# Kernel optimization log

Measured on AMD Instinct MI355X. Metric: run time of the kernel, lower is better.

The kernel has to match this reference:

```python
import jax, jax.numpy as jnp
import numpy as np

B, D_IN, D_OUT, N_CACHE = 2048, 1024, 512, 50000


def setup_inputs() -> dict:
    key = jax.random.key(0)
    k1, k2, k3, k4, k5 = jax.random.split(key, 5)
    scale = 1.0 / np.sqrt(D_IN)
    return {
        "x": jax.random.normal(k1, (B, D_IN), dtype=jnp.float32),
        "W": jax.random.normal(k2, (D_OUT, D_IN), dtype=jnp.float32) * scale,
        "b": jax.random.normal(k3, (D_OUT,), dtype=jnp.float32) * 0.01,
        "cache_image_features": jax.random.normal(k4, (N_CACHE, D_OUT), dtype=jnp.float32),
        "cache_text_features": jax.random.normal(k5, (N_CACHE, D_OUT), dtype=jnp.float32),
        "beta": jnp.ones((1,), dtype=jnp.float32),
        "alpha": jnp.ones((1,), dtype=jnp.float32),
    }


def reference(x, W, b, cache_image_features, cache_text_features, beta, alpha):
    # projected_x = x @ W.T + b  -> [B, D_OUT]
    projected_x = jnp.einsum('bi,oi->bo', x, W) + b
    # similarity over cached image features -> [B, N_CACHE]
    similarity = jnp.einsum('bo,no->bn', projected_x, cache_image_features)
    weights = jax.nn.softmax(beta * similarity, axis=-1)
    # retrieve from cached text features -> [B, D_OUT]
    retrieved = jnp.einsum('bn,no->bo', weights, cache_text_features)
    return projected_x + alpha * retrieved
```

## Files before the change

kernel.cpp:

```cpp
#include <hip/hip_runtime.h>
#include <hip/hip_bf16.h>
#include <math.h>

typedef _Float16 f16;
typedef __attribute__((ext_vector_type(8))) _Float16 f16x8;
typedef __attribute__((ext_vector_type(4))) float f32x4;
typedef __attribute__((ext_vector_type(16))) float f32x16;
typedef __attribute__((ext_vector_type(4))) unsigned int u32x4;
typedef __attribute__((ext_vector_type(2))) unsigned int u32x2;

#define MFMA16(A, B, C) __builtin_amdgcn_mfma_f32_16x16x32_f16(A, B, C, 0, 0, 0)
#define MFMA32(A, B, C) __builtin_amdgcn_mfma_f32_32x32x16_f16(A, B, C, 0, 0, 0)
#define AS1 __attribute__((address_space(1)))
#define AS3 __attribute__((address_space(3)))

__device__ __forceinline__ void gld16(const char* g, char* l) {
  __builtin_amdgcn_global_load_lds((const AS1 void*)g, (AS3 void*)l, 16, 0, 0);
}

__device__ __forceinline__ unsigned pk2(float a, float b) {
  f16 x = (f16)a, y = (f16)b;
  unsigned short ux = __builtin_bit_cast(unsigned short, x);
  unsigned short uy = __builtin_bit_cast(unsigned short, y);
  return (unsigned)ux | ((unsigned)uy << 16);
}

namespace {
constexpr int kB = 2048;
constexpr int kNch = 16, kChunk = 3125, kNit = 98;
constexpr int kKRows = 50176;
constexpr int kVStride = 3200;
constexpr size_t WS_PROJ = 0;
constexpr size_t WS_QHI  = WS_PROJ + (size_t)2048 * 512 * 4;
constexpr size_t WS_M    = WS_QHI + (size_t)2048 * 512 * 2;
constexpr size_t WS_L    = WS_M + (size_t)kNch * kB * 4;
constexpr size_t WS_PV   = WS_L + (size_t)kNch * kB * 4;
constexpr size_t WS_K16  = WS_PV + (size_t)kNch * kB * 512 * 2;
constexpr size_t WS_VT   = WS_K16 + (size_t)kKRows * 512 * 2;
constexpr int LDS_K0 = 0, LDS_K1 = 33280;
constexpr int LDS_V0 = 66560, LDS_V1 = 99328;
constexpr int LDS_SXP = 132096;
constexpr int LDS_FAC = 148480;
constexpr int LDS_SZ  = 148992;
}

__global__ __launch_bounds__(256) void convk_kernel(const float* __restrict__ src,
                                                    f16* __restrict__ dst) {
  const size_t e = ((size_t)blockIdx.x * 256 + threadIdx.x) * 8;
  const int row = (int)(e >> 9);
  float4 a = make_float4(0.f, 0.f, 0.f, 0.f), b = a;
  if (row < 50000) {
    a = *(const float4*)(src + e);
    b = *(const float4*)(src + e + 4);
  }
  f16x8 h;
  h[0] = (f16)a.x; h[1] = (f16)a.y; h[2] = (f16)a.z; h[3] = (f16)a.w;
  h[4] = (f16)b.x; h[5] = (f16)b.y; h[6] = (f16)b.z; h[7] = (f16)b.w;
  *(f16x8*)(dst + e) = h;
}

__global__ __launch_bounds__(256) void transv_kernel(const float* __restrict__ Vf,
                                                     f16* __restrict__ Vt) {
  __shared__ float tile[64][65];
  const int kt = blockIdx.x, colt = blockIdx.y, ch = blockIdx.z;
  const int t = threadIdx.x;
  const int kbase = kt * 64, col0 = colt * 64;
  {
    const int key = t >> 2, cseg = (t & 3) * 16;
    const int kk = kbase + key;
    float4 v0 = make_float4(0.f, 0.f, 0.f, 0.f), v1 = v0, v2 = v0, v3 = v0;
    if (kk < kChunk) {
      const float* s = Vf + (size_t)(ch * kChunk + kk) * 512 + col0 + cseg;
      v0 = *(const float4*)(s);
      v1 = *(const float4*)(s + 4);
      v2 = *(const float4*)(s + 8);
      v3 = *(const float4*)(s + 12);
    }
    float* tr = &tile[key][cseg];
    tr[0] = v0.x;  tr[1] = v0.y;  tr[2] = v0.z;  tr[3] = v0.w;
    tr[4] = v1.x;  tr[5] = v1.y;  tr[6] = v1.z;  tr[7] = v1.w;
    tr[8] = v2.x;  tr[9] = v2.y;  tr[10] = v2.z; tr[11] = v2.w;
    tr[12] = v3.x; tr[13] = v3.y; tr[14] = v3.z; tr[15] = v3.w;
  }
  __syncthreads();
  {
    const int col = t >> 2, kw = (t & 3) * 16;
    f16x8 h0, h1;
    #pragma unroll
    for (int u = 0; u < 8; u++) h0[u] = (f16)tile[kw + u][col];
    #pragma unroll
    for (int u = 0; u < 8; u++) h1[u] = (f16)tile[kw + 8 + u][col];
    f16* d = Vt + ((size_t)ch * 512 + col0 + col) * kVStride + kbase + kw;
    *(f16x8*)(d) = h0;
    *(f16x8*)(d + 8) = h1;
  }
}

__global__ __launch_bounds__(256) void gemm1_kernel(
    const float* __restrict__ x, const float* __restrict__ W,
    const float* __restrict__ bias, float* __restrict__ proj,
    f16* __restrict__ qhi)
{
  __shared__ f16 xh[2][64][40], xl[2][64][40], wh[2][64][40], wl[2][64][40];
  const int t = threadIdx.x;
  const int lane = t & 63, w = t >> 6;
  const int wr = w >> 1, wc = w & 1;
  const int g = lane >> 4, j = lane & 15;
  const int m0 = blockIdx.x * 64, n0 = blockIdx.y * 64;
  const int srow = t >> 2;
  const int soff = (t & 3) * 8;

  const f32x4 fzero = {0.f, 0.f, 0.f, 0.f};
  f32x4 acc[2][2], acc2[2][2];
  #pragma unroll
  for (int a = 0; a < 2; a++)
    #pragma unroll
    for (int bb = 0; bb < 2; bb++) { acc[a][bb] = fzero; acc2[a][bb] = fzero; }

  auto stage = [&](int k0s, int buf) {
    const float* xs  = x + (size_t)(m0 + srow) * 1024 + k0s + soff;
    const float* wsr = W + (size_t)(n0 + srow) * 1024 + k0s + soff;
    f16x8 hx, lx, hw, lw;
    #pragma unroll
    for (int i = 0; i < 8; i++) {
      float v = xs[i];
      f16 h = (f16)v;
      hx[i] = h;
      lx[i] = (f16)((v - (float)h) * 2048.0f);
      float u = wsr[i];
      f16 hu = (f16)u;
      hw[i] = hu;
      lw[i] = (f16)((u - (float)hu) * 2048.0f);
    }
    *(f16x8*)&xh[buf][srow][soff] = hx;
    *(f16x8*)&xl[buf][srow][soff] = lx;
    *(f16x8*)&wh[buf][srow][soff] = hw;
    *(f16x8*)&wl[buf][srow][soff] = lw;
  };

  stage(0, 0);
  for (int ks = 0; ks < 32; ks++) {
    __syncthreads();
    if (ks < 31) stage((ks + 1) * 32, (ks + 1) & 1);
    const int buf = ks & 1;
    f16x8 ah[2], al[2], bh[2], bl[2];
    #pragma unroll
    for (int mf = 0; mf < 2; mf++) {
      const int r = wr * 32 + mf * 16 + j;
      ah[mf] = *(const f16x8*)&xh[buf][r][g * 8];
      al[mf] = *(const f16x8*)&xl[buf][r][g * 8];
      const int c = wc * 32 + mf * 16 + j;
      bh[mf] = *(const f16x8*)&wh[buf][c][g * 8];
      bl[mf] = *(const f16x8*)&wl[buf][c][g * 8];
    }
    #pragma unroll
    for (int mf = 0; mf < 2; mf++)
      #pragma unroll
      for (int nf = 0; nf < 2; nf++) {
        acc[mf][nf]  = MFMA16(ah[mf], bh[nf], acc[mf][nf]);
        acc2[mf][nf] = MFMA16(ah[mf], bl[nf], acc2[mf][nf]);
        acc2[mf][nf] = MFMA16(al[mf], bh[nf], acc2[mf][nf]);
      }
  }

  #pragma unroll
  for (int mf = 0; mf < 2; mf++)
    #pragma unroll
    for (int nf = 0; nf < 2; nf++)
      #pragma unroll
      for (int r = 0; r < 4; r++) {
        const int m = m0 + wr * 32 + mf * 16 + g * 4 + r;
        const int n = n0 + wc * 32 + nf * 16 + j;
        float p = acc[mf][nf][r] + acc2[mf][nf][r] * (1.0f / 2048.0f) + bias[n];
        proj[(size_t)m * 512 + n] = p;
        qhi[(size_t)m * 512 + n] = (f16)p;
      }
}

__global__ __launch_bounds__(512, 2) void attn_kernel(
    const f16* __restrict__ K16, const f16* __restrict__ Vt16,
    const f16* __restrict__ qhi_ws, const float* __restrict__ beta_p,
    float* __restrict__ m_part, float* __restrict__ l_part,
    f16* __restrict__ pvn)
{
  extern __shared__ char smem[];
  const int t = threadIdx.x, lane = t & 63, w = t >> 6;
  const int c = lane & 31, h = lane >> 5;
  const int qb = w & 3, dh = w >> 2;
  const int ch = blockIdx.x & 15, qt = blockIdx.x >> 4;
  const int q0 = qt * 128;
  const float beta = beta_p[0];

  char* const Kb0 = smem + LDS_K0;
  char* const Kb1 = smem + LDS_K1;
  char* const Vb0 = smem + LDS_V0;
  char* const Vb1 = smem + LDS_V1;
  char* const SxP = smem + LDS_SXP + qb * 4096;
  float* const facl = (float*)(smem + LDS_FAC);

  f16x8 Qf[16];
  {
    const f16* qsrc = qhi_ws + (size_t)(q0 + qb * 32 + c) * 512 + dh * 256 + h * 8;
    #pragma unroll
    for (int i = 0; i < 16; i++) Qf[i] = *(const f16x8*)(qsrc + i * 16);
  }

  const char* const Kg = (const char*)K16 + (size_t)(ch * kChunk) * 1024;
  const char* const Vg = (const char*)Vt16 + (size_t)ch * 512 * (kVStride * 2);
  const int vlo = (((lane & 3) ^ ((lane >> 2) & 3)) << 4);

  auto stageK = [&](int it, char* dstbuf) {
    const char* src = Kg + (size_t)(it * 32 + w * 4) * 1024 + lane * 16;
    char* dst = dstbuf + (w * 4) * 1040 + lane * 16;
    #pragma unroll
    for (int u = 0; u < 4; u++) gld16(src + u * 1024, dst + u * 1040);
  };
  auto stageV = [&](int it, char* dstbuf) {
    const char* src = Vg + (size_t)(w * 64 + (lane >> 2)) * (kVStride * 2) + it * 64 + vlo;
    char* dst = dstbuf + (w * 64) * 64 + lane * 16;
    #pragma unroll
    for (int u = 0; u < 4; u++)
      gld16(src + (size_t)(u * 16) * (kVStride * 2), dst + u * 1024);
  };

  const int kroff = c * 1040 + dh * 512 + h * 16;
  const int vroff0 = (dh * 256 + c) * 64 + ((h * 16) ^ ((c & 3) << 4));
  const int vroff1 = (dh * 256 + c) * 64 + ((32 + h * 16) ^ ((c & 3) << 4));

  f32x16 O[8];
  #pragma unroll
  for (int nf = 0; nf < 8; nf++)
    #pragma unroll
    for (int r = 0; r < 16; r++) O[nf][r] = 0.f;
  float mrow = -INFINITY, lrow = 0.f;

  stageK(0, Kb0);
  stageV(0, Vb0);
  asm volatile("s_waitcnt vmcnt(0)" ::: "memory");
  __builtin_amdgcn_s_barrier();

  for (int it = 0; it < kNit; it++) {
    const int p = it & 1;
    char* const Kp = p ? Kb1 : Kb0;
    char* const Vp = p ? Vb1 : Vb0;
    if (it + 1 < kNit) {
      stageK(it + 1, p ? Kb0 : Kb1);
      stageV(it + 1, p ? Vb0 : Vb1);
    }

    f32x16 S;
    #pragma unroll
    for (int r = 0; r < 16; r++) S[r] = 0.f;
    const char* ka = Kp + kroff;
    __builtin_amdgcn_s_setprio(1);
    #pragma unroll
    for (int i = 0; i < 16; i++) {
      f16x8 a = *(const f16x8*)(ka + i * 32);
      S = MFMA32(a, Qf[i], S);
    }
    __builtin_amdgcn_s_setprio(0);

    if (dh == 1) {
      f32x4 v0 = {S[0], S[1], S[2], S[3]};
      f32x4 v1 = {S[4], S[5], S[6], S[7]};
      f32x4 v2 = {S[8], S[9], S[10], S[11]};
      f32x4 v3 = {S[12], S[13], S[14], S[15]};
      *(f32x4*)(SxP + 0 * 1024 + lane * 16) = v0;
      *(f32x4*)(SxP + 1 * 1024 + lane * 16) = v1;
      *(f32x4*)(SxP + 2 * 1024 + lane * 16) = v2;
      *(f32x4*)(SxP + 3 * 1024 + lane * 16) = v3;
    }
    asm volatile("s_waitcnt lgkmcnt(0)" ::: "memory");
    __builtin_amdgcn_s_barrier();

    u32x4 B0, B1;
    float fc;
    if (dh == 0) {
      #pragma unroll
      for (int cc = 0; cc < 4; cc++) {
        f32x4 v = *(const f32x4*)(SxP + cc * 1024 + lane * 16);
        S[4 * cc + 0] += v.x; S[4 * cc + 1] += v.y;
        S[4 * cc + 2] += v.z; S[4 * cc + 3] += v.w;
      }
      #pragma unroll
      for (int r = 0; r < 16; r++) S[r] *= beta;
      if (it == kNit - 1) {
        #pragma unroll
        for (int r = 0; r < 16; r++) {
          const int key = it * 32 + (r & 3) + 8 * (r >> 2) + 4 * h;
          if (key >= kChunk) S[r] = -INFINITY;
        }
      }
      float pm = S[0];
      #pragma unroll
      for (int r = 1; r < 16; r++) pm = fmaxf(pm, S[r]);
      pm = fmaxf(pm, __shfl_xor(pm, 32));
      const float mn = fmaxf(mrow, pm);
      fc = __expf(mrow - mn);
      mrow = mn;
      float pr[16], rs = 0.f;
      #pragma unroll
      for (int r = 0; r < 16; r++) { pr[r] = __expf(S[r] - mn); rs += pr[r]; }
      rs += __shfl_xor(rs, 32);
      lrow = lrow * fc + rs;
      unsigned pA0 = pk2(pr[0], pr[1]),  pA1 = pk2(pr[2], pr[3]);
      unsigned pB0 = pk2(pr[4], pr[5]),  pB1 = pk2(pr[6], pr[7]);
      unsigned pC0 = pk2(pr[8], pr[9]),  pC1 = pk2(pr[10], pr[11]);
      unsigned pD0 = pk2(pr[12], pr[13]), pD1 = pk2(pr[14], pr[15]);
      unsigned sA0 = __shfl_xor(pA0, 32), sA1 = __shfl_xor(pA1, 32);
      unsigned sB0 = __shfl_xor(pB0, 32), sB1 = __shfl_xor(pB1, 32);
      unsigned sC0 = __shfl_xor(pC0, 32), sC1 = __shfl_xor(pC1, 32);
      unsigned sD0 = __shfl_xor(pD0, 32), sD1 = __shfl_xor(pD1, 32);
      B0[0] = h ? sB0 : pA0;  B0[1] = h ? sB1 : pA1;
      B0[2] = h ? pB0 : sA0;  B0[3] = h ? pB1 : sA1;
      B1[0] = h ? sD0 : pC0;  B1[1] = h ? sD1 : pC1;
      B1[2] = h ? pD0 : sC0;  B1[3] = h ? pD1 : sC1;
      *(u32x4*)(SxP + 0 * 1024 + lane * 16) = B0;
      *(u32x4*)(SxP + 1 * 1024 + lane * 16) = B1;
      if (h == 0) facl[qb * 32 + c] = fc;
      #pragma unroll
      for (int nf = 0; nf < 8; nf++)
        #pragma unroll
        for (int r = 0; r < 16; r++) O[nf][r] *= fc;
    }
    asm volatile("s_waitcnt lgkmcnt(0)" ::: "memory");
    __builtin_amdgcn_s_barrier();
    if (dh == 1) {
      B0 = *(const u32x4*)(SxP + 0 * 1024 + lane * 16);
      B1 = *(const u32x4*)(SxP + 1 * 1024 + lane * 16);
      fc = facl[qb * 32 + c];
      #pragma unroll
      for (int nf = 0; nf < 8; nf++)
        #pragma unroll
        for (int r = 0; r < 16; r++) O[nf][r] *= fc;
    }

    const f16x8 pb0 = __builtin_bit_cast(f16x8, B0);
    const f16x8 pb1 = __builtin_bit_cast(f16x8, B1);
    __builtin_amdgcn_s_setprio(1);
    #pragma unroll
    for (int cf = 0; cf < 8; cf++) {
      f16x8 a0 = *(const f16x8*)(Vp + vroff0 + cf * 2048);
      f16x8 a1 = *(const f16x8*)(Vp + vroff1 + cf * 2048);
      O[cf] = MFMA32(a0, pb0, O[cf]);
      O[cf] = MFMA32(a1, pb1, O[cf]);
    }
    __builtin_amdgcn_s_setprio(0);

    asm volatile("s_waitcnt vmcnt(0)" ::: "memory");
    __builtin_amdgcn_s_barrier();
  }

  float iv = 0.f;
  if (dh == 0) {
    iv = 1.0f / lrow;
    if (lane < 32) {
      m_part[ch * kB + q0 + qb * 32 + c] = mrow;
      l_part[ch * kB + q0 + qb * 32 + c] = lrow;
      facl[qb * 32 + c] = iv;
    }
  }
  asm volatile("s_waitcnt lgkmcnt(0)" ::: "memory");
  __builtin_amdgcn_s_barrier();
  if (dh == 1) iv = facl[qb * 32 + c];

  const size_t prow = ((size_t)ch * kB + q0 + qb * 32 + c) * 512;
  #pragma unroll
  for (int cf = 0; cf < 8; cf++) {
    const int C = dh * 256 + cf * 32;
    #pragma unroll
    for (int a = 0; a < 4; a++) {
      unsigned lo = pk2(O[cf][4 * a + 0] * iv, O[cf][4 * a + 1] * iv);
      unsigned hi = pk2(O[cf][4 * a + 2] * iv, O[cf][4 * a + 3] * iv);
      u32x2 v = {lo, hi};
      *(u32x2*)(pvn + prow + C + 8 * a + 4 * h) = v;
    }
  }
}

__global__ __launch_bounds__(256) void combine_kernel(
    const float* __restrict__ proj, const float* __restrict__ m_part,
    const float* __restrict__ l_part, const f16* __restrict__ pvn,
    const float* __restrict__ alpha_p, float* __restrict__ out)
{
  const int row = blockIdx.x;
  const int t = threadIdx.x;
  const float alpha = alpha_p[0];
  float M = -INFINITY;
  #pragma unroll
  for (int c = 0; c < kNch; c++) M = fmaxf(M, m_part[c * kB + row]);
  float gl[kNch];
  float T = 0.f;
  #pragma unroll
  for (int c = 0; c < kNch; c++) {
    gl[c] = __expf(m_part[c * kB + row] - M) * l_part[c * kB + row];
    T += gl[c];
  }
  const float s = alpha / T;
  #pragma unroll
  for (int half = 0; half < 2; half++) {
    const int col = t + half * 256;
    float acc = 0.f;
    #pragma unroll
    for (int c = 0; c < kNch; c++)
      acc += gl[c] * (float)pvn[((size_t)c * kB + row) * 512 + col];
    out[(size_t)row * 512 + col] = proj[(size_t)row * 512 + col] + acc * s;
  }
}

extern "C" void kernel_launch(void* const* d_in, const int* in_sizes, int n_in,
                              void* d_out, int out_size, void* d_ws, size_t ws_size,
                              hipStream_t stream) {
  (void)in_sizes; (void)n_in; (void)out_size; (void)ws_size;
  const float* x     = (const float*)d_in[0];
  const float* W     = (const float*)d_in[1];
  const float* bias  = (const float*)d_in[2];
  const float* cimg  = (const float*)d_in[3];
  const float* ctxt  = (const float*)d_in[4];
  const float* beta  = (const float*)d_in[5];
  const float* alpha = (const float*)d_in[6];
  float* out = (float*)d_out;
  char* ws = (char*)d_ws;

  float* proj = (float*)(ws + WS_PROJ);
  f16*   qhi  = (f16*)(ws + WS_QHI);
  float* mp   = (float*)(ws + WS_M);
  float* lp   = (float*)(ws + WS_L);
  f16*   pvn  = (f16*)(ws + WS_PV);
  f16*   K16  = (f16*)(ws + WS_K16);
  f16*   Vt16 = (f16*)(ws + WS_VT);

  hipFuncSetAttribute((const void*)attn_kernel,
                      hipFuncAttributeMaxDynamicSharedMemorySize, LDS_SZ);

  convk_kernel<<<(kKRows * 512 / 8 + 255) / 256, 256, 0, stream>>>(cimg, K16);
  transv_kernel<<<dim3(kVStride / 64, 8, kNch), 256, 0, stream>>>(ctxt, Vt16);
  gemm1_kernel<<<dim3(32, 8), 256, 0, stream>>>(x, W, bias, proj, qhi);
  attn_kernel<<<256, 512, LDS_SZ, stream>>>(K16, Vt16, qhi, beta, mp, lp, pvn);
  combine_kernel<<<2048, 256, 0, stream>>>(proj, mp, lp, pvn, alpha, out);
}
```

Baseline: 408.8 us.

## Retile PV stage over query pairs and skip rescale via lazy max threshold

Each warp now computes PV for two query blocks and a 128-column slice of the output, so each V fragment loaded from LDS feeds two query blocks instead of one. The V swizzle pattern is changed to match the new access layout. The online softmax now only updates the running max and rescales O when some row's new max exceeds the old one by more than 8, and signals this through per-block LDS flags. This removes most rescale multiplies, but unnormalised probabilities can reach e^8 in fp16, which trades some precision headroom for less work.

```diff
diff --git a/kernel.cpp b/kernel.cpp
--- a/kernel.cpp
+++ b/kernel.cpp
@@ -41,7 +41,8 @@
 constexpr int LDS_V0 = 66560, LDS_V1 = 99328;
 constexpr int LDS_SXP = 132096;
 constexpr int LDS_FAC = 148480;
-constexpr int LDS_SZ  = 148992;
+constexpr int LDS_FLG = 148992;
+constexpr int LDS_SZ  = 149504;
 }
 
 __global__ __launch_bounds__(256) void convk_kernel(const float* __restrict__ src,
@@ -149,9 +150,9 @@
       const int r = wr * 32 + mf * 16 + j;
       ah[mf] = *(const f16x8*)&xh[buf][r][g * 8];
       al[mf] = *(const f16x8*)&xl[buf][r][g * 8];
-      const int c = wc * 32 + mf * 16 + j;
-      bh[mf] = *(const f16x8*)&wh[buf][c][g * 8];
-      bl[mf] = *(const f16x8*)&wl[buf][c][g * 8];
+      const int cc = wc * 32 + mf * 16 + j;
+      bh[mf] = *(const f16x8*)&wh[buf][cc][g * 8];
+      bl[mf] = *(const f16x8*)&wl[buf][cc][g * 8];
     }
     #pragma unroll
     for (int mf = 0; mf < 2; mf++)
@@ -187,6 +188,7 @@
   const int t = threadIdx.x, lane = t & 63, w = t >> 6;
   const int c = lane & 31, h = lane >> 5;
   const int qb = w & 3, dh = w >> 2;
+  const int qp = w & 1, cq = w >> 1;
   const int ch = blockIdx.x & 15, qt = blockIdx.x >> 4;
   const int q0 = qt * 128;
   const float beta = beta_p[0];
@@ -195,8 +197,9 @@
   char* const Kb1 = smem + LDS_K1;
   char* const Vb0 = smem + LDS_V0;
   char* const Vb1 = smem + LDS_V1;
-  char* const SxP = smem + LDS_SXP + qb * 4096;
+  char* const SxPq = smem + LDS_SXP + qb * 4096;
   float* const facl = (float*)(smem + LDS_FAC);
+  int* const flg = (int*)(smem + LDS_FLG);
 
   f16x8 Qf[16];
   {
@@ -204,10 +207,11 @@
     #pragma unroll
     for (int i = 0; i < 16; i++) Qf[i] = *(const f16x8*)(qsrc + i * 16);
   }
+  __builtin_amdgcn_sched_barrier(0);
 
   const char* const Kg = (const char*)K16 + (size_t)(ch * kChunk) * 1024;
   const char* const Vg = (const char*)Vt16 + (size_t)ch * 512 * (kVStride * 2);
-  const int vlo = (((lane & 3) ^ ((lane >> 2) & 3)) << 4);
+  const int vlo = (((lane & 3) ^ ((lane >> 3) & 3)) << 4);
 
   auto stageK = [&](int it, char* dstbuf) {
     const char* src = Kg + (size_t)(it * 32 + w * 4) * 1024 + lane * 16;
@@ -224,14 +228,20 @@
   };
 
   const int kroff = c * 1040 + dh * 512 + h * 16;
-  const int vroff0 = (dh * 256 + c) * 64 + ((h * 16) ^ ((c & 3) << 4));
-  const int vroff1 = (dh * 256 + c) * 64 + ((32 + h * 16) ^ ((c & 3) << 4));
-
-  f32x16 O[8];
-  #pragma unroll
-  for (int nf = 0; nf < 8; nf++)
-    #pragma unroll
-    for (int r = 0; r < 16; r++) O[nf][r] = 0.f;
+  const int vbase = (cq * 128 + c) * 64;
+  const int vswz = ((c >> 1) & 3) << 4;
+  const int voff0 = (0 + h * 16) ^ vswz;
+  const int voff1 = (32 + h * 16) ^ vswz;
+  const char* const slotA = smem + LDS_SXP + (2 * qp) * 4096 + lane * 16;
+  const char* const slotB = smem + LDS_SXP + (2 * qp + 1) * 4096 + lane * 16;
+
+  f32x16 O[2][4];
+  #pragma unroll
+  for (int ql = 0; ql < 2; ql++)
+    #pragma unroll
+    for (int cb = 0; cb < 4; cb++)
+      #pragma unroll
+      for (int r = 0; r < 16; r++) O[ql][cb][r] = 0.f;
   float mrow = -INFINITY, lrow = 0.f;
 
   stageK(0, Kb0);
@@ -241,8 +251,8 @@
 
   for (int it = 0; it < kNit; it++) {
     const int p = it & 1;
-    char* const Kp = p ? Kb1 : Kb0;
-    char* const Vp = p ? Vb1 : Vb0;
+    const char* const Kp = (p ? Kb1 : Kb0) + kroff;
+    const char* const Vp = (p ? Vb1 : Vb0) + vbase;
     if (it + 1 < kNit) {
       stageK(it + 1, p ? Kb0 : Kb1);
       stageV(it + 1, p ? Vb0 : Vb1);
@@ -251,11 +261,10 @@
     f32x16 S;
     #pragma unroll
     for (int r = 0; r < 16; r++) S[r] = 0.f;
-    const char* ka = Kp + kroff;
     __builtin_amdgcn_s_setprio(1);
     #pragma unroll
     for (int i = 0; i < 16; i++) {
-      f16x8 a = *(const f16x8*)(ka + i * 32);
+      f16x8 a = *(const f16x8*)(Kp + i * 32);
       S = MFMA32(a, Qf[i], S);
     }
     __builtin_amdgcn_s_setprio(0);
@@ -265,20 +274,18 @@
       f32x4 v1 = {S[4], S[5], S[6], S[7]};
       f32x4 v2 = {S[8], S[9], S[10], S[11]};
       f32x4 v3 = {S[12], S[13], S[14], S[15]};
-      *(f32x4*)(SxP + 0 * 1024 + lane * 16) = v0;
-      *(f32x4*)(SxP + 1 * 1024 + lane * 16) = v1;
-      *(f32x4*)(SxP + 2 * 1024 + lane * 16) = v2;
-      *(f32x4*)(SxP + 3 * 1024 + lane * 16) = v3;
+      *(f32x4*)(SxPq + 0 * 1024 + lane * 16) = v0;
+      *(f32x4*)(SxPq + 1 * 1024 + lane * 16) = v1;
+      *(f32x4*)(SxPq + 2 * 1024 + lane * 16) = v2;
+      *(f32x4*)(SxPq + 3 * 1024 + lane * 16) = v3;
     }
     asm volatile("s_waitcnt lgkmcnt(0)" ::: "memory");
     __builtin_amdgcn_s_barrier();
 
-    u32x4 B0, B1;
-    float fc;
     if (dh == 0) {
       #pragma unroll
       for (int cc = 0; cc < 4; cc++) {
-        f32x4 v = *(const f32x4*)(SxP + cc * 1024 + lane * 16);
+        f32x4 v = *(const f32x4*)(SxPq + cc * 1024 + lane * 16);
         S[4 * cc + 0] += v.x; S[4 * cc + 1] += v.y;
         S[4 * cc + 2] += v.z; S[4 * cc + 3] += v.w;
       }
@@ -295,12 +302,16 @@
       #pragma unroll
       for (int r = 1; r < 16; r++) pm = fmaxf(pm, S[r]);
       pm = fmaxf(pm, __shfl_xor(pm, 32));
-      const float mn = fmaxf(mrow, pm);
-      fc = __expf(mrow - mn);
-      mrow = mn;
+      const int need = __any(pm > mrow + 8.0f);
+      float fc = 1.0f;
+      if (need) {
+        const float mn = fmaxf(mrow, pm);
+        fc = __expf(mrow - mn);
+        mrow = mn;
+      }
       float pr[16], rs = 0.f;
       #pragma unroll
-      for (int r = 0; r < 16; r++) { pr[r] = __expf(S[r] - mn); rs += pr[r]; }
+      for (int r = 0; r < 16; r++) { pr[r] = __expf(S[r] - mrow); rs += pr[r]; }
       rs += __shfl_xor(rs, 32);
       lrow = lrow * fc + rs;
       unsigned pA0 = pk2(pr[0], pr[1]),  pA1 = pk2(pr[2], pr[3]);
@@ -311,39 +322,48 @@
       unsigned sB0 = __shfl_xor(pB0, 32), sB1 = __shfl_xor(pB1, 32);
       unsigned sC0 = __shfl_xor(pC0, 32), sC1 = __shfl_xor(pC1, 32);
       unsigned sD0 = __shfl_xor(pD0, 32), sD1 = __shfl_xor(pD1, 32);
+      u32x4 B0, B1;
       B0[0] = h ? sB0 : pA0;  B0[1] = h ? sB1 : pA1;
       B0[2] = h ? pB0 : sA0;  B0[3] = h ? pB1 : sA1;
       B1[0] = h ? sD0 : pC0;  B1[1] = h ? sD1 : pC1;
       B1[2] = h ? pD0 : sC0;  B1[3] = h ? pD1 : sC1;
-      *(u32x4*)(SxP + 0 * 1024 + lane * 16) = B0;
-      *(u32x4*)(SxP + 1 * 1024 + lane * 16) = B1;
-      if (h == 0) facl[qb * 32 + c] = fc;
-      #pragma unroll
-      for (int nf = 0; nf < 8; nf++)
-        #pragma unroll
-        for (int r = 0; r < 16; r++) O[nf][r] *= fc;
+      *(u32x4*)(SxPq + 0 * 1024 + lane * 16) = B0;
+      *(u32x4*)(SxPq + 1 * 1024 + lane * 16) = B1;
+      if (need && h == 0) facl[qb * 32 + c] = fc;
+      if (lane == 0) flg[qb] = need;
     }
     asm volatile("s_waitcnt lgkmcnt(0)" ::: "memory");
     __builtin_amdgcn_s_barrier();
-    if (dh == 1) {
-      B0 = *(const u32x4*)(SxP + 0 * 1024 + lane * 16);
-      B1 = *(const u32x4*)(SxP + 1 * 1024 + lane * 16);
-      fc = facl[qb * 32 + c];
-      #pragma unroll
-      for (int nf = 0; nf < 8; nf++)
+
+    const int f0 = flg[2 * qp];
+    const int f1 = flg[2 * qp + 1];
+    const f16x8 pb00 = *(const f16x8*)(slotA);
+    const f16x8 pb01 = *(const f16x8*)(slotA + 1024);
+    const f16x8 pb10 = *(const f16x8*)(slotB);
+    const f16x8 pb11 = *(const f16x8*)(slotB + 1024);
+    if (f0) {
+      const float fc0 = facl[(2 * qp) * 32 + c];
+      #pragma unroll
+      for (int cb = 0; cb < 4; cb++)
         #pragma unroll
-        for (int r = 0; r < 16; r++) O[nf][r] *= fc;
-    }
-
-    const f16x8 pb0 = __builtin_bit_cast(f16x8, B0);
-    const f16x8 pb1 = __builtin_bit_cast(f16x8, B1);
+        for (int r = 0; r < 16; r++) O[0][cb][r] *= fc0;
+    }
+    if (f1) {
+      const float fc1 = facl[(2 * qp + 1) * 32 + c];
+      #pragma unroll
+      for (int cb = 0; cb < 4; cb++)
+        #pragma unroll
+        for (int r = 0; r < 16; r++) O[1][cb][r] *= fc1;
+    }
     __builtin_amdgcn_s_setprio(1);
     #pragma unroll
-    for (int cf = 0; cf < 8; cf++) {
-      f16x8 a0 = *(const f16x8*)(Vp + vroff0 + cf * 2048);
-      f16x8 a1 = *(const f16x8*)(Vp + vroff1 + cf * 2048);
-      O[cf] = MFMA32(a0, pb0, O[cf]);
-      O[cf] = MFMA32(a1, pb1, O[cf]);
+    for (int cb = 0; cb < 4; cb++) {
+      f16x8 a0 = *(const f16x8*)(Vp + cb * 2048 + voff0);
+      f16x8 a1 = *(const f16x8*)(Vp + cb * 2048 + voff1);
+      O[0][cb] = MFMA32(a0, pb00, O[0][cb]);
+      O[0][cb] = MFMA32(a1, pb01, O[0][cb]);
+      O[1][cb] = MFMA32(a0, pb10, O[1][cb]);
+      O[1][cb] = MFMA32(a1, pb11, O[1][cb]);
     }
     __builtin_amdgcn_s_setprio(0);
 
@@ -351,9 +371,8 @@
     __builtin_amdgcn_s_barrier();
   }
 
-  float iv = 0.f;
   if (dh == 0) {
-    iv = 1.0f / lrow;
+    const float iv = 1.0f / lrow;
     if (lane < 32) {
       m_part[ch * kB + q0 + qb * 32 + c] = mrow;
       l_part[ch * kB + q0 + qb * 32 + c] = lrow;
@@ -362,18 +381,24 @@
   }
   asm volatile("s_waitcnt lgkmcnt(0)" ::: "memory");
   __builtin_amdgcn_s_barrier();
-  if (dh == 1) iv = facl[qb * 32 + c];
-
-  const size_t prow = ((size_t)ch * kB + q0 + qb * 32 + c) * 512;
-  #pragma unroll
-  for (int cf = 0; cf < 8; cf++) {
-    const int C = dh * 256 + cf * 32;
-    #pragma unroll
-    for (int a = 0; a < 4; a++) {
-      unsigned lo = pk2(O[cf][4 * a + 0] * iv, O[cf][4 * a + 1] * iv);
-      unsigned hi = pk2(O[cf][4 * a + 2] * iv, O[cf][4 * a + 3] * iv);
-      u32x2 v = {lo, hi};
-      *(u32x2*)(pvn + prow + C + 8 * a + 4 * h) = v;
+  const float iv0 = facl[(2 * qp) * 32 + c];
+  const float iv1 = facl[(2 * qp + 1) * 32 + c];
+
+  const size_t pvb = ((size_t)ch * kB + q0) * 512;
+  #pragma unroll
+  for (int ql = 0; ql < 2; ql++) {
+    const int qrow = (2 * qp + ql) * 32 + c;
+    const float iv = ql ? iv1 : iv0;
+    #pragma unroll
+    for (int cb = 0; cb < 4; cb++) {
+      const int C = cq * 128 + cb * 32;
+      #pragma unroll
+      for (int a = 0; a < 4; a++) {
+        unsigned lo = pk2(O[ql][cb][4 * a + 0] * iv, O[ql][cb][4 * a + 1] * iv);
+        unsigned hi = pk2(O[ql][cb][4 * a + 2] * iv, O[ql][cb][4 * a + 3] * iv);
+        u32x2 v = {lo, hi};
+        *(u32x2*)(pvn + pvb + (size_t)qrow * 512 + C + 8 * a + 4 * h) = v;
+      }
     }
   }
 }
```

Result: faster. 388.3 us (-5.0%).
